# Kernel optimization log

Measured on AMD Instinct MI355X. Metric: run time of the kernel, lower is better.

## Reference

```python
import jax, jax.numpy as jnp
import numpy as np

# loss coefficients (init_kwargs loss_coef_dict)
COEF_CLS = 1.0
COEF_REG = 1.0
COEF_CPT = 0.01


def setup_inputs() -> dict:
    key = jax.random.key(0)
    k1, k2, k3, k4, k5 = jax.random.split(key, 5)
    B, NCLS, K, H, W = 128, 200, 312, 28, 28
    return {
        "class_scores": jax.random.normal(k1, (B, NCLS), dtype=jnp.float32),
        "attr_scores_pred": jax.random.normal(k2, (B, K), dtype=jnp.float32),
        "attr_scores_gt": jax.random.uniform(k3, (B, K), dtype=jnp.float32),
        "attn_maps": jax.random.uniform(k4, (B, K, H, W), dtype=jnp.float32),
        "class_ids": jax.random.randint(k5, (B,), 0, NCLS, dtype=jnp.int64),
    }


def _l_cpt(attn_maps):
    # attn_maps: [b, k, h, w]; per-map argmax location, distance-weighted mean
    b, k, h, w = attn_maps.shape
    maps = attn_maps.reshape(b * k, h, w)
    flat_idx = jnp.argmax(maps.reshape(b * k, h * w), axis=-1)  # [bk]
    ch = (flat_idx // w).astype(attn_maps.dtype)  # row of max
    cw = (flat_idx % w).astype(attn_maps.dtype)   # col of max
    rows = jnp.arange(h, dtype=attn_maps.dtype)[None, :, None]  # grid_h
    cols = jnp.arange(w, dtype=attn_maps.dtype)[None, None, :]  # grid_w
    dist2 = (rows - ch[:, None, None]) ** 2 + (cols - cw[:, None, None]) ** 2
    per_map = jnp.mean(maps * dist2, axis=(1, 2))  # [bk]
    return jnp.mean(per_map)


def reference(class_scores, attr_scores_pred, attr_scores_gt, attn_maps, class_ids):
    # l_cls: mean cross-entropy
    logp = jax.nn.log_softmax(class_scores, axis=-1)
    l_cls = -jnp.mean(jnp.take_along_axis(logp, class_ids[:, None], axis=-1))
    # l_reg: mean squared error
    l_reg = jnp.mean((attr_scores_pred - attr_scores_gt) ** 2)
    # l_cpt: concentration loss
    l_cpt = _l_cpt(attn_maps)
    l_cls = COEF_CLS * l_cls
    l_reg = COEF_REG * l_reg
    l_cpt = COEF_CPT * l_cpt
    l_total = l_cls + l_reg + l_cpt
    return jnp.stack([l_cls, l_reg, l_cpt, l_total])
```

## Files before the change

### kernel.cpp

```cpp
#include <hip/hip_runtime.h>
#include <math.h>

#define BATCH   128
#define NCLS    200
#define KATTR   312
#define MH      28
#define MW      28
#define NMAPS   (BATCH * KATTR)
#define MAP_ELEMS (MH * MW)
#define MAP_GROUPS (MAP_ELEMS / 4)
#define NREG    (BATCH * KATTR)

#define MAPS_PER_WAVE   8
#define WAVES_PER_BLOCK 4
#define MAPS_PER_BLOCK  (MAPS_PER_WAVE * WAVES_PER_BLOCK)
#define CPT_BLOCKS      (NMAPS / MAPS_PER_BLOCK)
#define CLS_BLOCKS      (BATCH / WAVES_PER_BLOCK)
#define REG_BLOCKS      8
#define TOTAL_BLOCKS    (CPT_BLOCKS + CLS_BLOCKS + REG_BLOCKS)

#define WS_CLS  0
#define WS_REG  (WS_CLS + BATCH)
#define WS_CPT  (WS_REG + REG_BLOCKS)
#define WS_TOTAL (WS_CPT + CPT_BLOCKS)

#define COEF_CLS 1.0f
#define COEF_REG 1.0f
#define COEF_CPT 0.01f

__global__ __launch_bounds__(256) void apn_main(
    const float* __restrict__ class_scores,
    const float* __restrict__ pred,
    const float* __restrict__ gt,
    const float* __restrict__ attn,
    const int*   __restrict__ class_ids,
    float* __restrict__ ws)
{
    const int tid  = threadIdx.x;
    const int lane = tid & 63;
    const int wave = tid >> 6;
    const int blk  = blockIdx.x;

    __shared__ float lds[WAVES_PER_BLOCK];

    if (blk < CPT_BLOCKS) {
        const int m0 = blk * MAPS_PER_BLOCK + wave * MAPS_PER_WAVE;
        float wsum = 0.0f;

        for (int mm = 0; mm < MAPS_PER_WAVE; ++mm) {
            const float4* __restrict__ p4 =
                (const float4*)(attn + (size_t)(m0 + mm) * MAP_ELEMS);

            float4 v[4];
            float maxv = -INFINITY;
            int   maxi = 0;

            #pragma unroll
            for (int t = 0; t < 4; ++t) {
                const int g = lane + 64 * t;
                if (g < MAP_GROUPS) {
                    float4 x = p4[g];
                    v[t] = x;
                    const int bidx = g * 4;
                    if (x.x > maxv) { maxv = x.x; maxi = bidx;     }
                    if (x.y > maxv) { maxv = x.y; maxi = bidx + 1; }
                    if (x.z > maxv) { maxv = x.z; maxi = bidx + 2; }
                    if (x.w > maxv) { maxv = x.w; maxi = bidx + 3; }
                }
            }

            #pragma unroll
            for (int off = 1; off < 64; off <<= 1) {
                float ov = __shfl_xor(maxv, off);
                int   oi = __shfl_xor(maxi, off);
                if (ov > maxv || (ov == maxv && oi < maxi)) { maxv = ov; maxi = oi; }
            }

            const float chf = (float)(maxi / MW);
            const float cwf = (float)(maxi % MW);

            #pragma unroll
            for (int t = 0; t < 4; ++t) {
                const int g = lane + 64 * t;
                if (g < MAP_GROUPS) {
                    const int bidx = g * 4;
                    const float4 x = v[t];
                    {
                        int idx = bidx;     int h = idx / MW; int w = idx - h * MW;
                        float dh = (float)h - chf, dw = (float)w - cwf;
                        wsum += x.x * (dh * dh + dw * dw);
                    }
                    {
                        int idx = bidx + 1; int h = idx / MW; int w = idx - h * MW;
                        float dh = (float)h - chf, dw = (float)w - cwf;
                        wsum += x.y * (dh * dh + dw * dw);
                    }
                    {
                        int idx = bidx + 2; int h = idx / MW; int w = idx - h * MW;
                        float dh = (float)h - chf, dw = (float)w - cwf;
                        wsum += x.z * (dh * dh + dw * dw);
                    }
                    {
                        int idx = bidx + 3; int h = idx / MW; int w = idx - h * MW;
                        float dh = (float)h - chf, dw = (float)w - cwf;
                        wsum += x.w * (dh * dh + dw * dw);
                    }
                }
            }
        }

        #pragma unroll
        for (int off = 1; off < 64; off <<= 1) wsum += __shfl_xor(wsum, off);
        if (lane == 0) lds[wave] = wsum;
        __syncthreads();
        if (tid == 0) ws[WS_CPT + blk] = lds[0] + lds[1] + lds[2] + lds[3];

    } else if (blk < CPT_BLOCKS + CLS_BLOCKS) {
        const int row = (blk - CPT_BLOCKS) * WAVES_PER_BLOCK + wave;
        const float* __restrict__ xr = class_scores + (size_t)row * NCLS;

        float xv[4];
        float m = -INFINITY;
        #pragma unroll
        for (int t = 0; t < 4; ++t) {
            const int c = lane + 64 * t;
            if (c < NCLS) { xv[t] = xr[c]; m = fmaxf(m, xv[t]); }
            else            xv[t] = -INFINITY;
        }
        #pragma unroll
        for (int off = 1; off < 64; off <<= 1) m = fmaxf(m, __shfl_xor(m, off));

        float se = 0.0f;
        #pragma unroll
        for (int t = 0; t < 4; ++t) {
            const int c = lane + 64 * t;
            if (c < NCLS) se += expf(xv[t] - m);
        }
        #pragma unroll
        for (int off = 1; off < 64; off <<= 1) se += __shfl_xor(se, off);

        if (lane == 0) {
            const int cid = class_ids[row];
            const float lse = m + logf(se);
            ws[WS_CLS + row] = lse - xr[cid];
        }

    } else {
        const int rb = blk - CPT_BLOCKS - CLS_BLOCKS;
        const float4* __restrict__ p = (const float4*)pred;
        const float4* __restrict__ q = (const float4*)gt;
        float s = 0.0f;
        for (int i = rb * 256 + tid; i < NREG / 4; i += REG_BLOCKS * 256) {
            const float4 a = p[i];
            const float4 b = q[i];
            const float dx = a.x - b.x, dy = a.y - b.y, dz = a.z - b.z, dw = a.w - b.w;
            s += dx * dx + dy * dy + dz * dz + dw * dw;
        }
        #pragma unroll
        for (int off = 1; off < 64; off <<= 1) s += __shfl_xor(s, off);
        if (lane == 0) lds[wave] = s;
        __syncthreads();
        if (tid == 0) ws[WS_REG + rb] = lds[0] + lds[1] + lds[2] + lds[3];
    }
}

__global__ __launch_bounds__(256) void apn_final(
    const float* __restrict__ ws, float* __restrict__ out)
{
    const int tid  = threadIdx.x;
    const int lane = tid & 63;
    const int wave = tid >> 6;

    float a = 0.0f, b = 0.0f, c = 0.0f;
    for (int i = tid; i < BATCH; i += 256)      a += ws[WS_CLS + i];
    if (tid < REG_BLOCKS)                       b  = ws[WS_REG + tid];
    for (int i = tid; i < CPT_BLOCKS; i += 256) c += ws[WS_CPT + i];

    #pragma unroll
    for (int off = 1; off < 64; off <<= 1) {
        a += __shfl_xor(a, off);
        b += __shfl_xor(b, off);
        c += __shfl_xor(c, off);
    }

    __shared__ float la[4], lb[4], lc[4];
    if (lane == 0) { la[wave] = a; lb[wave] = b; lc[wave] = c; }
    __syncthreads();
    if (tid == 0) {
        const float sa = la[0] + la[1] + la[2] + la[3];
        const float sb = lb[0] + lb[1] + lb[2] + lb[3];
        const float sc = lc[0] + lc[1] + lc[2] + lc[3];
        const float l_cls = COEF_CLS * (sa / (float)BATCH);
        const float l_reg = COEF_REG * (sb / (float)NREG);
        const float l_cpt = COEF_CPT * (sc / ((float)NMAPS * (float)MAP_ELEMS));
        out[0] = l_cls;
        out[1] = l_reg;
        out[2] = l_cpt;
        out[3] = l_cls + l_reg + l_cpt;
    }
}

extern "C" void kernel_launch(void* const* d_in, const int* in_sizes, int n_in,
                              void* d_out, int out_size, void* d_ws, size_t ws_size,
                              hipStream_t stream) {
    const float* class_scores = (const float*)d_in[0];
    const float* pred         = (const float*)d_in[1];
    const float* gt           = (const float*)d_in[2];
    const float* attn         = (const float*)d_in[3];
    const int*   class_ids    = (const int*)d_in[4];
    float* ws  = (float*)d_ws;
    float* out = (float*)d_out;

    apn_main<<<dim3(TOTAL_BLOCKS), dim3(256), 0, stream>>>(
        class_scores, pred, gt, attn, class_ids, ws);
    apn_final<<<dim3(1), dim3(256), 0, stream>>>(ws, out);
}
```

Before: 193.6 us.

## Software-pipeline attention map loads with nontemporal prefetch and precomputed coordinates

```diff
diff --git a/kernel.cpp b/kernel.cpp
--- a/kernel.cpp
+++ b/kernel.cpp
@@ -17,7 +17,8 @@
 #define CPT_BLOCKS      (NMAPS / MAPS_PER_BLOCK)
 #define CLS_BLOCKS      (BATCH / WAVES_PER_BLOCK)
 #define REG_BLOCKS      8
-#define TOTAL_BLOCKS    (CPT_BLOCKS + CLS_BLOCKS + REG_BLOCKS)
+#define HEAD_BLOCKS     (CLS_BLOCKS + REG_BLOCKS)
+#define TOTAL_BLOCKS    (CPT_BLOCKS + HEAD_BLOCKS)
 
 #define WS_CLS  0
 #define WS_REG  (WS_CLS + BATCH)
@@ -27,6 +28,15 @@
 #define COEF_CLS 1.0f
 #define COEF_REG 1.0f
 #define COEF_CPT 0.01f
+
+#define ELEM(v4, j) ((j) == 0 ? (v4).x : (j) == 1 ? (v4).y : (j) == 2 ? (v4).z : (v4).w)
+
+typedef float v4f __attribute__((ext_vector_type(4)));
+
+__device__ __forceinline__ float4 ldnt(const float4* p) {
+    const v4f r = __builtin_nontemporal_load((const v4f*)p);
+    return make_float4(r.x, r.y, r.z, r.w);
+}
 
 __global__ __launch_bounds__(256) void apn_main(
     const float* __restrict__ class_scores,
@@ -43,36 +53,61 @@
 
     __shared__ float lds[WAVES_PER_BLOCK];
 
-    if (blk < CPT_BLOCKS) {
-        const int m0 = blk * MAPS_PER_BLOCK + wave * MAPS_PER_WAVE;
+    if (blk >= HEAD_BLOCKS) {
+        const int cb = blk - HEAD_BLOCKS;
+        const int m0 = cb * MAPS_PER_BLOCK + wave * MAPS_PER_WAVE;
+        const float4* __restrict__ base =
+            (const float4*)(attn + (size_t)m0 * MAP_ELEMS);
+
+        float hfv[4][4], wfv[4][4];
+        #pragma unroll
+        for (int t = 0; t < 4; ++t) {
+            #pragma unroll
+            for (int j = 0; j < 4; ++j) {
+                const int idx = (lane + 64 * t) * 4 + j;
+                const int h = idx / MW;
+                hfv[t][j] = (float)h;
+                wfv[t][j] = (float)(idx - h * MW);
+            }
+        }
+
+        const bool tail = (lane < (MAP_GROUPS - 192));
+        const float4 z4 = make_float4(0.f, 0.f, 0.f, 0.f);
+        const int lane4 = lane << 2;
+
+        float4 cur[4], nxt[4];
+
+        #pragma unroll
+        for (int t = 0; t < 3; ++t) cur[t] = ldnt(base + lane + 64 * t);
+        if (tail) cur[3] = ldnt(base + lane + 192); else cur[3] = z4;
+
         float wsum = 0.0f;
 
+        #pragma unroll
         for (int mm = 0; mm < MAPS_PER_WAVE; ++mm) {
-            const float4* __restrict__ p4 =
-                (const float4*)(attn + (size_t)(m0 + mm) * MAP_ELEMS);
-
-            float4 v[4];
+            if (mm + 1 < MAPS_PER_WAVE) {
+                const float4* __restrict__ bp = base + (size_t)(mm + 1) * MAP_GROUPS;
+                #pragma unroll
+                for (int t = 0; t < 3; ++t) nxt[t] = ldnt(bp + lane + 64 * t);
+                if (tail) nxt[3] = ldnt(bp + lane + 192); else nxt[3] = z4;
+            }
+
             float maxv = -INFINITY;
             int   maxi = 0;
-
             #pragma unroll
             for (int t = 0; t < 4; ++t) {
-                const int g = lane + 64 * t;
-                if (g < MAP_GROUPS) {
-                    float4 x = p4[g];
-                    v[t] = x;
-                    const int bidx = g * 4;
-                    if (x.x > maxv) { maxv = x.x; maxi = bidx;     }
-                    if (x.y > maxv) { maxv = x.y; maxi = bidx + 1; }
-                    if (x.z > maxv) { maxv = x.z; maxi = bidx + 2; }
-                    if (x.w > maxv) { maxv = x.w; maxi = bidx + 3; }
+                #pragma unroll
+                for (int j = 0; j < 4; ++j) {
+                    const float v = ELEM(cur[t], j);
+                    const int idx = lane4 + t * 256 + j;
+                    if (v > maxv) { maxv = v; maxi = idx; }
                 }
             }
 
             #pragma unroll
             for (int off = 1; off < 64; off <<= 1) {
-                float ov = __shfl_xor(maxv, off);
-                int   oi = __shfl_xor(maxi, off);
+                const float ov = __shfl_xor(maxv, off);
+                const int   oi = __shfl_xor(maxi, off);
                 if (ov > maxv || (ov == maxv && oi < maxi)) { maxv = ov; maxi = oi; }
             }
 
@@ -81,31 +116,17 @@
 
             #pragma unroll
             for (int t = 0; t < 4; ++t) {
-                const int g = lane + 64 * t;
-                if (g < MAP_GROUPS) {
-                    const int bidx = g * 4;
-                    const float4 x = v[t];
-                    {
-                        int idx = bidx;     int h = idx / MW; int w = idx - h * MW;
-                        float dh = (float)h - chf, dw = (float)w - cwf;
-                        wsum += x.x * (dh * dh + dw * dw);
-                    }
-                    {
-                        int idx = bidx + 1; int h = idx / MW; int w = idx - h * MW;
-                        float dh = (float)h - chf, dw = (float)w - cwf;
-                        wsum += x.y * (dh * dh + dw * dw);
-                    }
-                    {
-                        int idx = bidx + 2; int h = idx / MW; int w = idx - h * MW;
-                        float dh = (float)h - chf, dw = (float)w - cwf;
-                        wsum += x.z * (dh * dh + dw * dw);
-                    }
-                    {
-                        int idx = bidx + 3; int h = idx / MW; int w = idx - h * MW;
-                        float dh = (float)h - chf, dw = (float)w - cwf;
-                        wsum += x.w * (dh * dh + dw * dw);
-                    }
+                #pragma unroll
+                for (int j = 0; j < 4; ++j) {
+                    const float dh = hfv[t][j] - chf;
+                    const float dw = wfv[t][j] - cwf;
+                    wsum += ELEM(cur[t], j) * (dh * dh + dw * dw);
                 }
+            }
+
+            if (mm + 1 < MAPS_PER_WAVE) {
+                #pragma unroll
+                for (int t = 0; t < 4; ++t) cur[t] = nxt[t];
             }
         }
 
@@ -113,10 +134,10 @@
         for (int off = 1; off < 64; off <<= 1) wsum += __shfl_xor(wsum, off);
         if (lane == 0) lds[wave] = wsum;
         __syncthreads();
-        if (tid == 0) ws[WS_CPT + blk] = lds[0] + lds[1] + lds[2] + lds[3];
-
-    } else if (blk < CPT_BLOCKS + CLS_BLOCKS) {
-        const int row = (blk - CPT_BLOCKS) * WAVES_PER_BLOCK + wave;
+        if (tid == 0) ws[WS_CPT + cb] = lds[0] + lds[1] + lds[2] + lds[3];
+
+    } else if (blk < CLS_BLOCKS) {
+        const int row = blk * WAVES_PER_BLOCK + wave;
         const float* __restrict__ xr = class_scores + (size_t)row * NCLS;
 
         float xv[4];
@@ -146,7 +167,7 @@
         }
 
     } else {
-        const int rb = blk - CPT_BLOCKS - CLS_BLOCKS;
+        const int rb = blk - CLS_BLOCKS;
         const float4* __restrict__ p = (const float4*)pred;
         const float4* __restrict__ q = (const float4*)gt;
         float s = 0.0f;
```

Result: faster. 187.7 us (-3.1%).
